# Optimization experiments

Hardware: AMD Instinct MI355X
Metric: run time of the kernel (lower is better)

The kernel has to match this reference:

```python
import jax, jax.numpy as jnp
import numpy as np
from jax import lax

D_MODEL = 768
EXPAND = 2
D_INNER = D_MODEL * EXPAND  # 1536
N_STATE = 16
DT_RANK = D_INNER // 16  # 96
K_CONV = 4
B, L = 2, 1024


def setup_inputs() -> dict:
    key = jax.random.key(0)
    ks = jax.random.split(key, 20)
    s = lambda i, shape, scale=0.02: jax.random.normal(ks[i], shape, dtype=jnp.float32) * scale
    # dt_proj bias init (inverse softplus of dt in [0.001, 0.1])
    def dt_bias(k):
        dt = jnp.exp(jax.random.uniform(k, (D_INNER,)) * (np.log(0.1) - np.log(0.001)) + np.log(0.001))
        return dt + jnp.log(-jnp.expm1(-dt))
    A_log = jnp.log(jnp.arange(1, N_STATE + 1, dtype=jnp.float32))[None, :] * jnp.ones((D_INNER, 1), jnp.float32)
    inp = {
        "u": jax.random.normal(ks[0], (B, L, D_MODEL), dtype=jnp.float32),
        "norm_w": jnp.ones((D_MODEL,), jnp.float32),
        "norm_b": jnp.zeros((D_MODEL,), jnp.float32),
        "fwd_in_w": s(1, (2 * D_INNER, D_MODEL)),
        "fwd_conv_w": s(2, (D_INNER, 1, K_CONV), 0.1),
        "fwd_conv_b": jnp.zeros((D_INNER,), jnp.float32),
        "fwd_A_log": A_log,
        "fwd_xproj_w": s(3, (DT_RANK + 2 * N_STATE, D_INNER)),
        "fwd_dt_w": s(4, (D_INNER, DT_RANK)),
        "fwd_dt_b": dt_bias(ks[5]),
        "fwd_D": jnp.ones((D_INNER,), jnp.float32),
        "bwd_in_w": s(6, (2 * D_INNER, D_MODEL)),
        "bwd_conv_w": s(7, (D_INNER, 1, K_CONV), 0.1),
        "bwd_conv_b": jnp.zeros((D_INNER,), jnp.float32),
        "bwd_A_log": A_log,
        "bwd_xproj_w": s(8, (DT_RANK + 2 * N_STATE, D_INNER)),
        "bwd_dt_w": s(9, (D_INNER, DT_RANK)),
        "bwd_dt_b": dt_bias(ks[10]),
        "bwd_D": jnp.ones((D_INNER,), jnp.float32),
        "out_w": s(11, (D_MODEL, 2 * D_INNER)),
    }
    return inp


def _layernorm(x, w, b, eps=1e-5):
    mu = jnp.mean(x, axis=-1, keepdims=True)
    var = jnp.mean(jnp.square(x - mu), axis=-1, keepdims=True)
    return (x - mu) * lax.rsqrt(var + eps) * w + b


def _dw_causal_conv(x, w, b):
    # x: (B, L, D); torch Conv1d(pad=k-1, groups=D) then trim to L == left-pad causal conv
    xc = jnp.transpose(x, (0, 2, 1))  # (B, D, L)
    y = lax.conv_general_dilated(xc, w, window_strides=(1,),
                                 padding=[(K_CONV - 1, 0)],
                                 feature_group_count=D_INNER,
                                 dimension_numbers=('NCH', 'OIH', 'NCH'))
    return jnp.transpose(y + b[None, :, None], (0, 2, 1))


def _ssm(x, A_log, xproj_w, dt_w, dt_b, Dp):
    # x: (B, L, D)
    x_dbl = x @ xproj_w.T  # (B, L, dt_rank + 2N)
    dt_raw = x_dbl[..., :DT_RANK]
    B_sel = x_dbl[..., DT_RANK:DT_RANK + N_STATE]   # (B, L, N)
    C_sel = x_dbl[..., DT_RANK + N_STATE:]           # (B, L, N)
    dt = jax.nn.softplus(dt_raw @ dt_w.T + dt_b)      # (B, L, D)
    A = -jnp.exp(A_log)                               # (D, N)
    A_bar = jnp.exp(dt[..., None] * A)                # (B, L, D, N)
    Bu = (dt * x)[..., None] * B_sel[:, :, None, :]   # (B, L, D, N)
    # linear recurrence h_t = A_bar_t * h_{t-1} + Bu_t via associative scan
    def combine(c1, c2):
        a1, b1 = c1
        a2, b2 = c2
        return a1 * a2, a2 * b1 + b2
    _, h = lax.associative_scan(combine, (A_bar, Bu), axis=1)
    y = jnp.einsum('bldn,bln->bld', h, C_sel)
    return y + x * Dp


def _branch(u, in_w, conv_w, conv_b, A_log, xproj_w, dt_w, dt_b, Dp, reverse):
    if reverse:
        u = u[:, ::-1]
    xz = u @ in_w.T
    x, z = xz[..., :D_INNER], xz[..., D_INNER:]
    x = jax.nn.silu(_dw_causal_conv(x, conv_w, conv_b))
    x = _ssm(x, A_log, xproj_w, dt_w, dt_b, Dp)
    x = x * jax.nn.silu(z)
    if reverse:
        x = x[:, ::-1]
    return x


def reference(u, norm_w, norm_b,
              fwd_in_w, fwd_conv_w, fwd_conv_b, fwd_A_log, fwd_xproj_w, fwd_dt_w, fwd_dt_b, fwd_D,
              bwd_in_w, bwd_conv_w, bwd_conv_b, bwd_A_log, bwd_xproj_w, bwd_dt_w, bwd_dt_b, bwd_D,
              out_w):
    residual = u
    un = _layernorm(u, norm_w, norm_b)
    x_fwd = _branch(un, fwd_in_w, fwd_conv_w, fwd_conv_b, fwd_A_log, fwd_xproj_w, fwd_dt_w, fwd_dt_b, fwd_D, False)
    x_bwd = _branch(un, bwd_in_w, bwd_conv_w, bwd_conv_b, bwd_A_log, bwd_xproj_w, bwd_dt_w, bwd_dt_b, bwd_D, True)
    x = jnp.concatenate([x_fwd, x_bwd], axis=-1) @ out_w.T
    return x + residual
```

## Files before the change

kernel.cpp:

```cpp
#include <hip/hip_runtime.h>
#include <hip/hip_bf16.h>

#define D_MODEL 768
#define D_INNER 1536
#define N_STATE 16
#define DT_RANK 96
#define KCONV   4
#define Bv      2
#define Lv      1024
#define MROWS   (Bv*Lv)
#define CH      128
#define G       (Lv/CH)
#define PADL    68

typedef __attribute__((ext_vector_type(8))) short bf16x8;
typedef __attribute__((ext_vector_type(4))) float f32x4;

__device__ __forceinline__ void gll16(const void* g, void* l) {
    __builtin_amdgcn_global_load_lds(
        (const __attribute__((address_space(1))) void*)g,
        (__attribute__((address_space(3))) void*)l, 16, 0, 0);
}

__device__ __forceinline__ unsigned short f2bf(float f) {
    unsigned u = __builtin_bit_cast(unsigned, f);
    u += 0x7fffu + ((u >> 16) & 1u);
    return (unsigned short)(u >> 16);
}

template<int CTRL>
__device__ __forceinline__ float dpp_ror_add(float v) {
    int vi = __builtin_bit_cast(int, v);
    int mv = __builtin_amdgcn_update_dpp(vi, vi, CTRL, 0xf, 0xf, true);
    return v + __builtin_bit_cast(float, mv);
}

__global__ __launch_bounds__(256)
void ln_kernel(const float* __restrict__ u, const float* __restrict__ w,
               const float* __restrict__ bvec, unsigned short* __restrict__ o)
{
    int row = blockIdx.x;
    const float* x = u + (size_t)row * D_MODEL;
    int t = threadIdx.x;
    float v0 = x[t], v1 = x[t + 256], v2 = x[t + 512];
    float s  = v0 + v1 + v2;
    float s2 = v0*v0 + v1*v1 + v2*v2;
    for (int off = 32; off; off >>= 1) {
        s  += __shfl_down(s, off);
        s2 += __shfl_down(s2, off);
    }
    __shared__ float rs[4], rs2[4];
    __shared__ float mu_s, rstd_s;
    int wid = t >> 6, lane = t & 63;
    if (lane == 0) { rs[wid] = s; rs2[wid] = s2; }
    __syncthreads();
    if (t == 0) {
        float S  = rs[0] + rs[1] + rs[2] + rs[3];
        float S2 = rs2[0] + rs2[1] + rs2[2] + rs2[3];
        float mu = S / (float)D_MODEL;
        float var = S2 / (float)D_MODEL - mu * mu;
        mu_s = mu;
        rstd_s = rsqrtf(var + 1e-5f);
    }
    __syncthreads();
    float mu = mu_s, r = rstd_s;
    unsigned short* orow = o + (size_t)row * D_MODEL;
    orow[t]       = f2bf((v0 - mu) * r * w[t]       + bvec[t]);
    orow[t + 256] = f2bf((v1 - mu) * r * w[t + 256] + bvec[t + 256]);
    orow[t + 512] = f2bf((v2 - mu) * r * w[t + 512] + bvec[t + 512]);
}

__global__ __launch_bounds__(256)
void f2b(const float* __restrict__ in, unsigned short* __restrict__ o, int n4)
{
    int i = blockIdx.x * 256 + threadIdx.x;
    if (i < n4) {
        float4 v = ((const float4*)in)[i];
        ushort4 r;
        r.x = f2bf(v.x); r.y = f2bf(v.y); r.z = f2bf(v.z); r.w = f2bf(v.w);
        ((ushort4*)o)[i] = r;
    }
}

__global__ __launch_bounds__(256)
void gemm_mfma(const unsigned short* __restrict__ A, int lda, int revA, int Lr,
               const unsigned short* __restrict__ W,
               const float* __restrict__ bias, int act,
               const float* __restrict__ res,
               float* __restrict__ C,
               int M, int N, int K)
{
    __shared__ unsigned short As[128 * 32];
    __shared__ unsigned short Bs[128 * 32];
    const int tid = threadIdx.x;
    const int m0 = blockIdx.y * 128, n0 = blockIdx.x * 128;
    const int lane = tid & 63;
    const int w  = tid >> 6;
    const int wr = w >> 1, wc = w & 1;
    const int lm = lane & 15, lk = lane >> 4;

    const int srow = tid >> 2;
    const int skq  = (tid & 3) * 8;
    int arow0 = m0 + srow, arow1 = m0 + srow + 64;
    if (revA) {
        arow0 = (arow0 / Lr) * Lr + (Lr - 1 - arow0 % Lr);
        arow1 = (arow1 / Lr) * Lr + (Lr - 1 - arow1 % Lr);
    }
    const unsigned short* a0 = A + (size_t)arow0 * lda + skq;
    const unsigned short* a1 = A + (size_t)arow1 * lda + skq;
    const unsigned short* w0 = W + (size_t)(n0 + srow) * K + skq;
    const unsigned short* w1 = W + (size_t)(n0 + srow + 64) * K + skq;

    f32x4 acc[4][4] = {};

    for (int k0 = 0; k0 < K; k0 += 32) {
        __syncthreads();
        gll16(a0 + k0, &As[tid * 8]);
        gll16(a1 + k0, &As[2048 + tid * 8]);
        gll16(w0 + k0, &Bs[tid * 8]);
        gll16(w1 + k0, &Bs[2048 + tid * 8]);
        __syncthreads();

        bf16x8 af[4], bfr[4];
        #pragma unroll
        for (int i = 0; i < 4; i++) {
            af[i]  = *(const bf16x8*)&As[(wr * 64 + i * 16 + lm) * 32 + lk * 8];
            bfr[i] = *(const bf16x8*)&Bs[(wc * 64 + i * 16 + lm) * 32 + lk * 8];
        }
        #pragma unroll
        for (int i = 0; i < 4; i++)
            #pragma unroll
            for (int j = 0; j < 4; j++)
                acc[i][j] = __builtin_amdgcn_mfma_f32_16x16x32_bf16(af[i], bfr[j], acc[i][j], 0, 0, 0);
    }

    #pragma unroll
    for (int i = 0; i < 4; i++) {
        #pragma unroll
        for (int j = 0; j < 4; j++) {
            int row = m0 + wr * 64 + i * 16 + lk * 4;
            int col = n0 + wc * 64 + j * 16 + lm;
            #pragma unroll
            for (int r = 0; r < 4; r++) {
                float v = acc[i][j][r];
                if (bias) v += bias[col];
                if (act == 2) v = (v > 20.f) ? v : log1pf(__expf(v));
                if (res)  v += res[(size_t)(row + r) * N + col];
                C[(size_t)(row + r) * N + col] = v;
            }
        }
    }
}

__global__ __launch_bounds__(256)
void conv_silu(const float* __restrict__ xz, const float* __restrict__ w,
               const float* __restrict__ bias, float* __restrict__ xo,
               unsigned short* __restrict__ xbf)
{
    int t  = blockIdx.x * 256 + threadIdx.x;
    int d  = t % D_INNER;
    int lc = (t / D_INNER) % (Lv / 8);
    int b  = t / (D_INNER * (Lv / 8));
    int l0 = lc * 8;
    const float* src = xz + (size_t)b * Lv * (2 * D_INNER) + d;
    float w0 = w[d*4], w1 = w[d*4+1], w2 = w[d*4+2], w3 = w[d*4+3];
    float bb = bias[d];
    float v[11];
    #pragma unroll
    for (int j = 0; j < 11; j++) {
        int l = l0 - 3 + j;
        v[j] = (l >= 0) ? src[(size_t)l * (2 * D_INNER)] : 0.f;
    }
    size_t base = ((size_t)b * Lv + l0) * D_INNER + d;
    #pragma unroll
    for (int j = 0; j < 8; j++) {
        float a = bb + w0*v[j] + w1*v[j+1] + w2*v[j+2] + w3*v[j+3];
        a = a / (1.f + __expf(-a));
        xo[base + (size_t)j * D_INNER] = a;
        xbf[base + (size_t)j * D_INNER] = f2bf(a);
    }
}

__global__ __launch_bounds__(128)
void scan1(const float* __restrict__ xF, float* __restrict__ dtF,
           const float* __restrict__ xdF, const float* __restrict__ AlF,
           const float* __restrict__ DFp,
           const float* __restrict__ xB, float* __restrict__ dtB,
           const float* __restrict__ xdB, const float* __restrict__ AlB,
           const float* __restrict__ DBp,
           float* __restrict__ y_loc, float* __restrict__ h_end)
{
    const int br = blockIdx.z;
    const int bb = blockIdx.y >> 3, g = blockIdx.y & 7;
    const int d0 = blockIdx.x * 8;

    const float* x    = br ? xB  : xF;
    float*       dtp  = br ? dtB : dtF;
    const float* xd   = br ? xdB : xdF;
    const float* Alog = br ? AlB : AlF;
    const float* Dp   = br ? DBp : DFp;

    __shared__ float xs [2][8][PADL];
    __shared__ float dls[2][8][PADL];
    __shared__ float Bss[2][16][PADL];
    __shared__ float Css[2][16][PADL];

    const int t = threadIdx.x;
    const int n = t & 15, dloc = t >> 4;

    const float* xg  = x   + ((size_t)bb * Lv + g * CH) * D_INNER + d0;
    float*       dtg = dtp + ((size_t)bb * Lv + g * CH) * D_INNER + d0;
    const float* bcg = xd  + ((size_t)bb * Lv + g * CH) * 128;

    const int sl = t >> 1, sdq = (t & 1) * 4;
    const int bl0 = t >> 2,         bq0 = (t & 3) * 4;
    const int bl1 = (t + 128) >> 2, bq1 = ((t + 128) & 3) * 4;

    f32x4 rx, rdt, rb0, rb1, rc0, rc1;

    #define LOADG1(c) do {                                                       \
        int l0_ = (c) * 64;                                                      \
        rx  = *(const f32x4*)(xg  + (size_t)(l0_ + sl) * D_INNER + sdq);         \
        rdt = *(const f32x4*)(dtg + (size_t)(l0_ + sl) * D_INNER + sdq);         \
        rb0 = *(const f32x4*)(bcg + (size_t)(l0_ + bl0) * 128 + DT_RANK           + bq0); \
        rb1 = *(const f32x4*)(bcg + (size_t)(l0_ + bl1) * 128 + DT_RANK           + bq1); \
        rc0 = *(const f32x4*)(bcg + (size_t)(l0_ + bl0) * 128 + DT_RANK + N_STATE + bq0); \
        rc1 = *(const f32x4*)(bcg + (size_t)(l0_ + bl1) * 128 + DT_RANK + N_STATE + bq1); \
    } while (0)

    #define WRITEL1(p) do {                                                      \
        _Pragma("unroll")                                                        \
        for (int j = 0; j < 4; j++) {                                            \
            xs [p][sdq+j][sl] = rx[j];                                           \
            dls[p][sdq+j][sl] = rdt[j];                                          \
            Bss[p][bq0+j][bl0] = rb0[j];                                         \
            Bss[p][bq1+j][bl1] = rb1[j];                                         \
            Css[p][bq0+j][bl0] = rc0[j];                                         \
            Css[p][bq1+j][bl1] = rc1[j];                                         \
        }                                                                        \
    } while (0)

    const float An = -__expf(Alog[(d0 + dloc) * N_STATE + n]);
    const float Dd = Dp[d0 + dloc];
    float h = 0.f, srun = 0.f;

    LOADG1(0);
    WRITEL1(0);
    __syncthreads();

    for (int c = 0; c < 2; ++c) {
        const int p = c;
        if (c == 0) LOADG1(1);

        float yq[4] = {}, Sq[4] = {};
        #pragma unroll
        for (int gg = 0; gg < 16; ++gg) {
            f32x4 xv  = *(const f32x4*)&xs [p][dloc][gg*4];
            f32x4 dtv = *(const f32x4*)&dls[p][dloc][gg*4];
            f32x4 bv  = *(const f32x4*)&Bss[p][n][gg*4];
            f32x4 cv  = *(const f32x4*)&Css[p][n][gg*4];
            #pragma unroll
            for (int j = 0; j < 4; ++j) {
                const int l = gg * 4 + j;
                float dtl = dtv[j];
                float ab = __expf(dtl * An);
                h = fmaf(ab, h, dtl * xv[j] * bv[j]);
                srun += dtl;
                float contrib = h * cv[j];
                contrib = dpp_ror_add<0x121>(contrib);
                contrib = dpp_ror_add<0x122>(contrib);
                contrib = dpp_ror_add<0x124>(contrib);
                contrib = dpp_ror_add<0x128>(contrib);
                float y = contrib + xv[j] * Dd;
                if ((l & 15) == n) { yq[l >> 4] = y; Sq[l >> 4] = srun; }
            }
        }
        if (c == 0) WRITEL1(1);

        #pragma unroll
        for (int q = 0; q < 4; ++q) {
            int lc2 = c * 64 + q * 16 + n;
            int gl  = g * CH + lc2;
            y_loc[((size_t)(br*Bv + bb) * Lv + gl) * D_INNER + d0 + dloc] = yq[q];
            dtg[(size_t)lc2 * D_INNER + dloc] = Sq[q];
        }
        __syncthreads();
    }
    h_end[(((size_t)(br*Bv + bb) * G + g) * D_INNER + d0 + dloc) * 16 + n] = h;
    #undef LOADG1
    #undef WRITEL1
}

__global__ __launch_bounds__(256)
void scan2(const float* __restrict__ SF, const float* __restrict__ SB,
           const float* __restrict__ AlF, const float* __restrict__ AlB,
           const float* __restrict__ h_end, float* __restrict__ h0buf)
{
    int idx = blockIdx.x * 256 + threadIdx.x;
    int n = idx & 15;
    int rest = idx >> 4;
    int d  = rest % D_INNER;
    int bbr = rest / D_INNER;
    int bb = bbr & 1, br = bbr >> 1;

    const float* S    = br ? SB  : SF;
    const float* Alog = br ? AlB : AlF;
    float An = -__expf(Alog[d * N_STATE + n]);

    float h0 = 0.f;
    #pragma unroll
    for (int g = 0; g < G; ++g) {
        size_t base = (((size_t)(br*Bv + bb) * G + g) * D_INNER + d) * 16 + n;
        h0buf[base] = h0;
        float Send = S[((size_t)bb * Lv + g * CH + CH - 1) * D_INNER + d];
        h0 = __expf(An * Send) * h0 + h_end[base];
    }
}

__global__ __launch_bounds__(128)
void scan3(const float* __restrict__ SF, const float* __restrict__ xdF,
           const float* __restrict__ xzF, const float* __restrict__ AlF,
           const float* __restrict__ SB, const float* __restrict__ xdB,
           const float* __restrict__ xzB, const float* __restrict__ AlB,
           const float* __restrict__ y_loc, const float* __restrict__ h0buf,
           unsigned short* __restrict__ ycat)
{
    const int br = blockIdx.z;
    const int bb = blockIdx.y >> 3, g = blockIdx.y & 7;
    const int d0 = blockIdx.x * 8;

    const float* S    = br ? SB  : SF;
    const float* xd   = br ? xdB : xdF;
    const float* xz   = br ? xzB : xzF;
    const float* Alog = br ? AlB : AlF;

    __shared__ float Ss [2][8][PADL];
    __shared__ float zs [2][8][PADL];
    __shared__ float ys [2][8][PADL];
    __shared__ float Css[2][16][PADL];

    const int t = threadIdx.x;
    const int n = t & 15, dloc = t >> 4;

    const float* Sg  = S  + ((size_t)bb * Lv + g * CH) * D_INNER + d0;
    const float* zg  = xz + ((size_t)bb * Lv + g * CH) * (2*D_INNER) + D_INNER + d0;
    const float* yg  = y_loc + ((size_t)(br*Bv + bb) * Lv + g * CH) * D_INNER + d0;
    const float* bcg = xd + ((size_t)bb * Lv + g * CH) * 128;

    const int sl = t >> 1, sdq = (t & 1) * 4;
    const int bl0 = t >> 2,         bq0 = (t & 3) * 4;
    const int bl1 = (t + 128) >> 2, bq1 = ((t + 128) & 3) * 4;

    f32x4 rS, rz, ry, rc0, rc1;

    #define LOADG3(c) do {                                                       \
        int l0_ = (c) * 64;                                                      \
        rS = *(const f32x4*)(Sg + (size_t)(l0_ + sl) * D_INNER + sdq);           \
        rz = *(const f32x4*)(zg + (size_t)(l0_ + sl) * (2*D_INNER) + sdq);       \
        ry = *(const f32x4*)(yg + (size_t)(l0_ + sl) * D_INNER + sdq);           \
        rc0 = *(const f32x4*)(bcg + (size_t)(l0_ + bl0) * 128 + DT_RANK + N_STATE + bq0); \
        rc1 = *(const f32x4*)(bcg + (size_t)(l0_ + bl1) * 128 + DT_RANK + N_STATE + bq1); \
    } while (0)

    #define WRITEL3(p) do {                                                      \
        _Pragma("unroll")                                                        \
        for (int j = 0; j < 4; j++) {                                            \
            Ss[p][sdq+j][sl] = rS[j];                                            \
            zs[p][sdq+j][sl] = rz[j];                                            \
            ys[p][sdq+j][sl] = ry[j];                                            \
            Css[p][bq0+j][bl0] = rc0[j];                                         \
            Css[p][bq1+j][bl1] = rc1[j];                                         \
        }                                                                        \
    } while (0)

    const float An = -__expf(Alog[(d0 + dloc) * N_STATE + n]);
    const float h0 = h0buf[(((size_t)(br*Bv + bb) * G + g) * D_INNER + d0 + dloc) * 16 + n];

    LOADG3(0);
    WRITEL3(0);
    __syncthreads();

    for (int c = 0; c < 2; ++c) {
        const int p = c;
        if (c == 0) LOADG3(1);

        float yq[4] = {};
        #pragma unroll
        for (int gg = 0; gg < 16; ++gg) {
            f32x4 Sv = *(const f32x4*)&Ss [p][dloc][gg*4];
            f32x4 zv = *(const f32x4*)&zs [p][dloc][gg*4];
            f32x4 yv = *(const f32x4*)&ys [p][dloc][gg*4];
            f32x4 cv = *(const f32x4*)&Css[p][n][gg*4];
            #pragma unroll
            for (int j = 0; j < 4; ++j) {
                const int l = gg * 4 + j;
                float corr = cv[j] * __expf(An * Sv[j]) * h0;
                corr = dpp_ror_add<0x121>(corr);
                corr = dpp_ror_add<0x122>(corr);
                corr = dpp_ror_add<0x124>(corr);
                corr = dpp_ror_add<0x128>(corr);
                float y = yv[j] + corr;
                y *= zv[j] * __builtin_amdgcn_rcpf(1.f + __expf(-zv[j]));
                if ((l & 15) == n) yq[l >> 4] = y;
            }
        }
        if (c == 0) WRITEL3(1);

        #pragma unroll
        for (int q = 0; q < 4; ++q) {
            int gl = g * CH + c * 64 + q * 16 + n;
            int lo = br ? (Lv - 1 - gl) : gl;
            ycat[((size_t)bb * Lv + lo) * (2*D_INNER) + br * D_INNER + d0 + dloc] = f2bf(yq[q]);
        }
        __syncthreads();
    }
    #undef LOADG3
    #undef WRITEL3
}

extern "C" void kernel_launch(void* const* d_in, const int* in_sizes, int n_in,
                              void* d_out, int out_size, void* d_ws, size_t ws_size,
                              hipStream_t stream)
{
    (void)in_sizes; (void)n_in; (void)out_size; (void)ws_size;
    const float* u        = (const float*)d_in[0];
    const float* norm_w   = (const float*)d_in[1];
    const float* norm_b   = (const float*)d_in[2];
    const float* f_in_w   = (const float*)d_in[3];
    const float* f_conv_w = (const float*)d_in[4];
    const float* f_conv_b = (const float*)d_in[5];
    const float* f_Alog   = (const float*)d_in[6];
    const float* f_xproj  = (const float*)d_in[7];
    const float* f_dt_w   = (const float*)d_in[8];
    const float* f_dt_b   = (const float*)d_in[9];
    const float* f_D      = (const float*)d_in[10];
    const float* b_in_w   = (const float*)d_in[11];
    const float* b_conv_w = (const float*)d_in[12];
    const float* b_conv_b = (const float*)d_in[13];
    const float* b_Alog   = (const float*)d_in[14];
    const float* b_xproj  = (const float*)d_in[15];
    const float* b_dt_w   = (const float*)d_in[16];
    const float* b_dt_b   = (const float*)d_in[17];
    const float* b_D      = (const float*)d_in[18];
    const float* out_w    = (const float*)d_in[19];
    float* out = (float*)d_out;

    float* p = (float*)d_ws;
    unsigned short* un_bf = (unsigned short*)p;  p += (size_t)MROWS * D_MODEL;
    float* xz_f   = p;  p += (size_t)MROWS * 2 * D_INNER;
    float* xz_b   = p;  p += (size_t)MROWS * 2 * D_INNER;
    float* x_f    = p;  p += (size_t)MROWS * D_INNER;
    float* x_b    = p;  p += (size_t)MROWS * D_INNER;
    unsigned short* xbf_f = (unsigned short*)p;  p += (size_t)MROWS * D_INNER / 2;
    unsigned short* xbf_b = (unsigned short*)p;  p += (size_t)MROWS * D_INNER / 2;
    float* xdbl_f = p;  p += (size_t)MROWS * 128;
    float* xdbl_b = p;  p += (size_t)MROWS * 128;
    float* dt_f   = p;  p += (size_t)MROWS * D_INNER;
    float* dt_b_  = p;  p += (size_t)MROWS * D_INNER;
    unsigned short* yc_bf = (unsigned short*)p;  p += (size_t)MROWS * D_INNER;
    unsigned short* fw_bf = (unsigned short*)p;  p += (size_t)D_INNER * D_MODEL;
    unsigned short* bw_bf = (unsigned short*)p;  p += (size_t)D_INNER * D_MODEL;
    unsigned short* xwf_bf = (unsigned short*)p; p += (size_t)64 * D_INNER;
    unsigned short* xwb_bf = (unsigned short*)p; p += (size_t)64 * D_INNER;
    unsigned short* ow_bf = (unsigned short*)p;  p += (size_t)D_MODEL * D_INNER;
    float* y_loc  = p;  p += (size_t)2 * MROWS * D_INNER;
    float* h_end  = p;  p += (size_t)2 * Bv * G * D_INNER * N_STATE;
    float* h0buf  = p;  p += (size_t)2 * Bv * G * D_INNER * N_STATE;
    unsigned short* xdbf_f = (unsigned short*)p; p += (size_t)MROWS * 128 / 2;
    unsigned short* xdbf_b = (unsigned short*)p; p += (size_t)MROWS * 128 / 2;
    unsigned short* dtwf_bf = (unsigned short*)p; p += (size_t)D_INNER * DT_RANK / 2;
    unsigned short* dtwb_bf = (unsigned short*)p; p += (size_t)D_INNER * DT_RANK / 2;

    ln_kernel<<<MROWS, 256, 0, stream>>>(u, norm_w, norm_b, un_bf);

    f2b<<<(2*D_INNER*D_MODEL/4 + 255)/256, 256, 0, stream>>>(f_in_w, fw_bf, 2*D_INNER*D_MODEL/4);
    f2b<<<(2*D_INNER*D_MODEL/4 + 255)/256, 256, 0, stream>>>(b_in_w, bw_bf, 2*D_INNER*D_MODEL/4);
    f2b<<<(128*D_INNER/4 + 255)/256, 256, 0, stream>>>(f_xproj, xwf_bf, 128*D_INNER/4);
    f2b<<<(128*D_INNER/4 + 255)/256, 256, 0, stream>>>(b_xproj, xwb_bf, 128*D_INNER/4);
    f2b<<<(D_MODEL*2*D_INNER/4 + 255)/256, 256, 0, stream>>>(out_w, ow_bf, D_MODEL*2*D_INNER/4);
    f2b<<<(D_INNER*DT_RANK/4 + 255)/256, 256, 0, stream>>>(f_dt_w, dtwf_bf, D_INNER*DT_RANK/4);
    f2b<<<(D_INNER*DT_RANK/4 + 255)/256, 256, 0, stream>>>(b_dt_w, dtwb_bf, D_INNER*DT_RANK/4);

    gemm_mfma<<<dim3(2*D_INNER/128, MROWS/128), 256, 0, stream>>>(
        un_bf, D_MODEL, 0, Lv, fw_bf, nullptr, 0, nullptr, xz_f, MROWS, 2*D_INNER, D_MODEL);
    gemm_mfma<<<dim3(2*D_INNER/128, MROWS/128), 256, 0, stream>>>(
        un_bf, D_MODEL, 1, Lv, bw_bf, nullptr, 0, nullptr, xz_b, MROWS, 2*D_INNER, D_MODEL);

    int convBlocks = (Bv * (Lv/8) * D_INNER) / 256;
    conv_silu<<<convBlocks, 256, 0, stream>>>(xz_f, f_conv_w, f_conv_b, x_f, xbf_f);
    conv_silu<<<convBlocks, 256, 0, stream>>>(xz_b, b_conv_w, b_conv_b, x_b, xbf_b);

    gemm_mfma<<<dim3(1, MROWS/128), 256, 0, stream>>>(
        xbf_f, D_INNER, 0, Lv, xwf_bf, nullptr, 0, nullptr, xdbl_f, MROWS, 128, D_INNER);
    gemm_mfma<<<dim3(1, MROWS/128), 256, 0, stream>>>(
        xbf_b, D_INNER, 0, Lv, xwb_bf, nullptr, 0, nullptr, xdbl_b, MROWS, 128, D_INNER);

    f2b<<<(MROWS*128/4 + 255)/256, 256, 0, stream>>>(xdbl_f, xdbf_f, MROWS*128/4);
    f2b<<<(MROWS*128/4 + 255)/256, 256, 0, stream>>>(xdbl_b, xdbf_b, MROWS*128/4);
    gemm_mfma<<<dim3(D_INNER/128, MROWS/128), 256, 0, stream>>>(
        xdbf_f, 128, 0, Lv, dtwf_bf, f_dt_b, 2, nullptr, dt_f, MROWS, D_INNER, DT_RANK);
    gemm_mfma<<<dim3(D_INNER/128, MROWS/128), 256, 0, stream>>>(
        xdbf_b, 128, 0, Lv, dtwb_bf, b_dt_b, 2, nullptr, dt_b_, MROWS, D_INNER, DT_RANK);

    scan1<<<dim3(D_INNER/8, Bv*G, 2), 128, 0, stream>>>(
        x_f, dt_f, xdbl_f, f_Alog, f_D,
        x_b, dt_b_, xdbl_b, b_Alog, b_D, y_loc, h_end);
    scan2<<<(2*Bv*D_INNER*N_STATE)/256, 256, 0, stream>>>(
        dt_f, dt_b_, f_Alog, b_Alog, h_end, h0buf);
    scan3<<<dim3(D_INNER/8, Bv*G, 2), 128, 0, stream>>>(
        dt_f, xdbl_f, xz_f, f_Alog,
        dt_b_, xdbl_b, xz_b, b_Alog, y_loc, h0buf, yc_bf);

    gemm_mfma<<<dim3(D_MODEL/128, MROWS/128), 256, 0, stream>>>(
        yc_bf, 2*D_INNER, 0, Lv, ow_bf, nullptr, 0, u, out, MROWS, D_MODEL, 2*D_INNER);
}
```

Baseline: 622.9 us.

## Recompute chunk scan in pass three instead of storing local outputs

```diff
diff --git a/kernel.cpp b/kernel.cpp
--- a/kernel.cpp
+++ b/kernel.cpp
@@ -181,67 +181,58 @@
     }
 }
 
-__global__ __launch_bounds__(128)
-void scan1(const float* __restrict__ xF, float* __restrict__ dtF,
+__global__ __launch_bounds__(128, 6)
+void scan1(const float* __restrict__ xF, const float* __restrict__ dtF,
            const float* __restrict__ xdF, const float* __restrict__ AlF,
-           const float* __restrict__ DFp,
-           const float* __restrict__ xB, float* __restrict__ dtB,
+           const float* __restrict__ xB, const float* __restrict__ dtB,
            const float* __restrict__ xdB, const float* __restrict__ AlB,
-           const float* __restrict__ DBp,
-           float* __restrict__ y_loc, float* __restrict__ h_end)
+           float* __restrict__ h_end, float* __restrict__ Send)
 {
     const int br = blockIdx.z;
     const int bb = blockIdx.y >> 3, g = blockIdx.y & 7;
     const int d0 = blockIdx.x * 8;
 
     const float* x    = br ? xB  : xF;
-    float*       dtp  = br ? dtB : dtF;
+    const float* dt   = br ? dtB : dtF;
     const float* xd   = br ? xdB : xdF;
     const float* Alog = br ? AlB : AlF;
-    const float* Dp   = br ? DBp : DFp;
 
     __shared__ float xs [2][8][PADL];
     __shared__ float dls[2][8][PADL];
     __shared__ float Bss[2][16][PADL];
-    __shared__ float Css[2][16][PADL];
 
     const int t = threadIdx.x;
     const int n = t & 15, dloc = t >> 4;
 
-    const float* xg  = x   + ((size_t)bb * Lv + g * CH) * D_INNER + d0;
-    float*       dtg = dtp + ((size_t)bb * Lv + g * CH) * D_INNER + d0;
-    const float* bcg = xd  + ((size_t)bb * Lv + g * CH) * 128;
+    const float* xg  = x  + ((size_t)bb * Lv + g * CH) * D_INNER + d0;
+    const float* dtg = dt + ((size_t)bb * Lv + g * CH) * D_INNER + d0;
+    const float* bcg = xd + ((size_t)bb * Lv + g * CH) * 128;
 
     const int sl = t >> 1, sdq = (t & 1) * 4;
     const int bl0 = t >> 2,         bq0 = (t & 3) * 4;
     const int bl1 = (t + 128) >> 2, bq1 = ((t + 128) & 3) * 4;
 
-    f32x4 rx, rdt, rb0, rb1, rc0, rc1;
+    f32x4 rx, rdt, rb0, rb1;
 
     #define LOADG1(c) do {                                                       \
         int l0_ = (c) * 64;                                                      \
         rx  = *(const f32x4*)(xg  + (size_t)(l0_ + sl) * D_INNER + sdq);         \
         rdt = *(const f32x4*)(dtg + (size_t)(l0_ + sl) * D_INNER + sdq);         \
-        rb0 = *(const f32x4*)(bcg + (size_t)(l0_ + bl0) * 128 + DT_RANK           + bq0); \
-        rb1 = *(const f32x4*)(bcg + (size_t)(l0_ + bl1) * 128 + DT_RANK           + bq1); \
-        rc0 = *(const f32x4*)(bcg + (size_t)(l0_ + bl0) * 128 + DT_RANK + N_STATE + bq0); \
-        rc1 = *(const f32x4*)(bcg + (size_t)(l0_ + bl1) * 128 + DT_RANK + N_STATE + bq1); \
+        rb0 = *(const f32x4*)(bcg + (size_t)(l0_ + bl0) * 128 + DT_RANK + bq0);  \
+        rb1 = *(const f32x4*)(bcg + (size_t)(l0_ + bl1) * 128 + DT_RANK + bq1);  \
     } while (0)
 
-    #define WRITEL1(p) do {                                                      \
-        _Pragma("unroll")                                                        \
-        for (int j = 0; j < 4; j++) {                                            \
-            xs [p][sdq+j][sl] = rx[j];                                           \
-            dls[p][sdq+j][sl] = rdt[j];                                          \
-            Bss[p][bq0+j][bl0] = rb0[j];                                         \
-            Bss[p][bq1+j][bl1] = rb1[j];                                         \
-            Css[p][bq0+j][bl0] = rc0[j];                                         \
-            Css[p][bq1+j][bl1] = rc1[j];                                         \
-        }                                                                        \
+    #define WRITEL1(p) do {                                                     \
+        _Pragma("unroll")                                                       \
+        for (int j = 0; j < 4; j++) {                                           \
+            xs [p][sdq+j][sl] = rx[j];                                          \
+            dls[p][sdq+j][sl] = rdt[j];                                         \
+            Bss[p][bq0+j][bl0] = rb0[j];                                        \
+            Bss[p][bq1+j][bl1] = rb1[j];                                        \
+        }                                                                       \
     } while (0)
 
     const float An = -__expf(Alog[(d0 + dloc) * N_STATE + n]);
-    const float Dd = Dp[d0 + dloc];
     float h = 0.f, srun = 0.f;
 
     LOADG1(0);
@@ -252,47 +243,30 @@
         const int p = c;
         if (c == 0) LOADG1(1);
 
-        float yq[4] = {}, Sq[4] = {};
         #pragma unroll
         for (int gg = 0; gg < 16; ++gg) {
             f32x4 xv  = *(const f32x4*)&xs [p][dloc][gg*4];
             f32x4 dtv = *(const f32x4*)&dls[p][dloc][gg*4];
             f32x4 bv  = *(const f32x4*)&Bss[p][n][gg*4];
-            f32x4 cv  = *(const f32x4*)&Css[p][n][gg*4];
             #pragma unroll
             for (int j = 0; j < 4; ++j) {
-                const int l = gg * 4 + j;
-                float dtl = dtv[j];
-                float ab = __expf(dtl * An);
-                h = fmaf(ab, h, dtl * xv[j] * bv[j]);
-                srun += dtl;
-                float contrib = h * cv[j];
-                contrib = dpp_ror_add<0x121>(contrib);
-                contrib = dpp_ror_add<0x122>(contrib);
-                contrib = dpp_ror_add<0x124>(contrib);
-                contrib = dpp_ror_add<0x128>(contrib);
-                float y = contrib + xv[j] * Dd;
-                if ((l & 15) == n) { yq[l >> 4] = y; Sq[l >> 4] = srun; }
+                float ab = __expf(dtv[j] * An);
+                h = fmaf(ab, h, dtv[j] * xv[j] * bv[j]);
+                srun += dtv[j];
             }
         }
-        if (c == 0) WRITEL1(1);
-
-        #pragma unroll
-        for (int q = 0; q < 4; ++q) {
-            int lc2 = c * 64 + q * 16 + n;
-            int gl  = g * CH + lc2;
-            y_loc[((size_t)(br*Bv + bb) * Lv + gl) * D_INNER + d0 + dloc] = yq[q];
-            dtg[(size_t)lc2 * D_INNER + dloc] = Sq[q];
-        }
+        if (c == 0) { WRITEL1(1); }
         __syncthreads();
     }
     h_end[(((size_t)(br*Bv + bb) * G + g) * D_INNER + d0 + dloc) * 16 + n] = h;
+    if (n == 0)
+        Send[((size_t)(br*Bv + bb) * G + g) * D_INNER + d0 + dloc] = srun;
     #undef LOADG1
     #undef WRITEL1
 }
 
 __global__ __launch_bounds__(256)
-void scan2(const float* __restrict__ SF, const float* __restrict__ SB,
+void scan2(const float* __restrict__ Send,
            const float* __restrict__ AlF, const float* __restrict__ AlB,
            const float* __restrict__ h_end, float* __restrict__ h0buf)
 {
@@ -303,7 +277,6 @@
     int bbr = rest / D_INNER;
     int bb = bbr & 1, br = bbr >> 1;
 
-    const float* S    = br ? SB  : SF;
     const float* Alog = br ? AlB : AlF;
     float An = -__expf(Alog[d * N_STATE + n]);
 
@@ -312,69 +285,78 @@
     for (int g = 0; g < G; ++g) {
         size_t base = (((size_t)(br*Bv + bb) * G + g) * D_INNER + d) * 16 + n;
         h0buf[base] = h0;
-        float Send = S[((size_t)bb * Lv + g * CH + CH - 1) * D_INNER + d];
-        h0 = __expf(An * Send) * h0 + h_end[base];
-    }
-}
-
-__global__ __launch_bounds__(128)
-void scan3(const float* __restrict__ SF, const float* __restrict__ xdF,
-           const float* __restrict__ xzF, const float* __restrict__ AlF,
-           const float* __restrict__ SB, const float* __restrict__ xdB,
-           const float* __restrict__ xzB, const float* __restrict__ AlB,
-           const float* __restrict__ y_loc, const float* __restrict__ h0buf,
-           unsigned short* __restrict__ ycat)
+        float Se = Send[((size_t)(br*Bv + bb) * G + g) * D_INNER + d];
+        h0 = __expf(An * Se) * h0 + h_end[base];
+    }
+}
+
+__global__ __launch_bounds__(128, 4)
+void scan3(const float* __restrict__ xF, const float* __restrict__ dtF,
+           const float* __restrict__ xdF, const float* __restrict__ xzF,
+           const float* __restrict__ AlF, const float* __restrict__ DFp,
+           const float* __restrict__ xB, const float* __restrict__ dtB,
+           const float* __restrict__ xdB, const float* __restrict__ xzB,
+           const float* __restrict__ AlB, const float* __restrict__ DBp,
+           const float* __restrict__ h0buf, unsigned short* __restrict__ ycat)
 {
     const int br = blockIdx.z;
     const int bb = blockIdx.y >> 3, g = blockIdx.y & 7;
     const int d0 = blockIdx.x * 8;
 
-    const float* S    = br ? SB  : SF;
+    const float* x    = br ? xB  : xF;
+    const float* dt   = br ? dtB : dtF;
     const float* xd   = br ? xdB : xdF;
     const float* xz   = br ? xzB : xzF;
     const float* Alog = br ? AlB : AlF;
-
-    __shared__ float Ss [2][8][PADL];
+    const float* Dp   = br ? DBp : DFp;
+
+    __shared__ float xs [2][8][PADL];
+    __shared__ float dls[2][8][PADL];
     __shared__ float zs [2][8][PADL];
-    __shared__ float ys [2][8][PADL];
+    __shared__ float Bss[2][16][PADL];
     __shared__ float Css[2][16][PADL];
 
     const int t = threadIdx.x;
     const int n = t & 15, dloc = t >> 4;
 
-    const float* Sg  = S  + ((size_t)bb * Lv + g * CH) * D_INNER + d0;
+    const float* xg  = x  + ((size_t)bb * Lv + g * CH) * D_INNER + d0;
+    const float* dtg = dt + ((size_t)bb * Lv + g * CH) * D_INNER + d0;
     const float* zg  = xz + ((size_t)bb * Lv + g * CH) * (2*D_INNER) + D_INNER + d0;
-    const float* yg  = y_loc + ((size_t)(br*Bv + bb) * Lv + g * CH) * D_INNER + d0;
     const float* bcg = xd + ((size_t)bb * Lv + g * CH) * 128;
 
     const int sl = t >> 1, sdq = (t & 1) * 4;
     const int bl0 = t >> 2,         bq0 = (t & 3) * 4;
     const int bl1 = (t + 128) >> 2, bq1 = ((t + 128) & 3) * 4;
 
-    f32x4 rS, rz, ry, rc0, rc1;
+    f32x4 rx, rdt, rz, rb0, rb1, rc0, rc1;
 
     #define LOADG3(c) do {                                                       \
         int l0_ = (c) * 64;                                                      \
-        rS = *(const f32x4*)(Sg + (size_t)(l0_ + sl) * D_INNER + sdq);           \
-        rz = *(const f32x4*)(zg + (size_t)(l0_ + sl) * (2*D_INNER) + sdq);       \
-        ry = *(const f32x4*)(yg + (size_t)(l0_ + sl) * D_INNER + sdq);           \
+        rx  = *(const f32x4*)(xg  + (size_t)(l0_ + sl) * D_INNER + sdq);         \
+        rdt = *(const f32x4*)(dtg + (size_t)(l0_ + sl) * D_INNER + sdq);         \
+        rz  = *(const f32x4*)(zg  + (size_t)(l0_ + sl) * (2*D_INNER) + sdq);     \
+        rb0 = *(const f32x4*)(bcg + (size_t)(l0_ + bl0) * 128 + DT_RANK           + bq0); \
+        rb1 = *(const f32x4*)(bcg + (size_t)(l0_ + bl1) * 128 + DT_RANK           + bq1); \
         rc0 = *(const f32x4*)(bcg + (size_t)(l0_ + bl0) * 128 + DT_RANK + N_STATE + bq0); \
         rc1 = *(const f32x4*)(bcg + (size_t)(l0_ + bl1) * 128 + DT_RANK + N_STATE + bq1); \
     } while (0)
 
-    #define WRITEL3(p) do {                                                      \
-        _Pragma("unroll")                                                        \
-        for (int j = 0; j < 4; j++) {                                            \
-            Ss[p][sdq+j][sl] = rS[j];                                            \
-            zs[p][sdq+j][sl] = rz[j];                                            \
-            ys[p][sdq+j][sl] = ry[j];                                            \
-            Css[p][bq0+j][bl0] = rc0[j];                                         \
-            Css[p][bq1+j][bl1] = rc1[j];                                         \
-        }                                                                        \
+    #define WRITEL3(p) do {                                                     \
+        _Pragma("unroll")                                                       \
+        for (int j = 0; j < 4; j++) {                                           \
+            xs [p][sdq+j][sl] = rx[j];                                          \
+            dls[p][sdq+j][sl] = rdt[j];                                         \
+            zs [p][sdq+j][sl] = rz[j];                                          \
+            Bss[p][bq0+j][bl0] = rb0[j];                                        \
+            Bss[p][bq1+j][bl1] = rb1[j];                                        \
+            Css[p][bq0+j][bl0] = rc0[j];                                        \
+            Css[p][bq1+j][bl1] = rc1[j];                                        \
+        }                                                                       \
     } while (0)
 
     const float An = -__expf(Alog[(d0 + dloc) * N_STATE + n]);
-    const float h0 = h0buf[(((size_t)(br*Bv + bb) * G + g) * D_INNER + d0 + dloc) * 16 + n];
+    const float Dd = Dp[d0 + dloc];
+    float h = h0buf[(((size_t)(br*Bv + bb) * G + g) * D_INNER + d0 + dloc) * 16 + n];
 
     LOADG3(0);
     WRITEL3(0);
@@ -387,24 +369,27 @@
         float yq[4] = {};
         #pragma unroll
         for (int gg = 0; gg < 16; ++gg) {
-            f32x4 Sv = *(const f32x4*)&Ss [p][dloc][gg*4];
-            f32x4 zv = *(const f32x4*)&zs [p][dloc][gg*4];
-            f32x4 yv = *(const f32x4*)&ys [p][dloc][gg*4];
-            f32x4 cv = *(const f32x4*)&Css[p][n][gg*4];
+            f32x4 xv  = *(const f32x4*)&xs [p][dloc][gg*4];
+            f32x4 dtv = *(const f32x4*)&dls[p][dloc][gg*4];
+            f32x4 zv  = *(const f32x4*)&zs [p][dloc][gg*4];
+            f32x4 bv  = *(const f32x4*)&Bss[p][n][gg*4];
+            f32x4 cv  = *(const f32x4*)&Css[p][n][gg*4];
             #pragma unroll
             for (int j = 0; j < 4; ++j) {
                 const int l = gg * 4 + j;
-                float corr = cv[j] * __expf(An * Sv[j]) * h0;
-                corr = dpp_ror_add<0x121>(corr);
-                corr = dpp_ror_add<0x122>(corr);
-                corr = dpp_ror_add<0x124>(corr);
-                corr = dpp_ror_add<0x128>(corr);
-                float y = yv[j] + corr;
-                y *= zv[j] * __builtin_amdgcn_rcpf(1.f + __expf(-zv[j]));
+                float ab = __expf(dtv[j] * An);
+                h = fmaf(ab, h, dtv[j] * xv[j] * bv[j]);
+                float contrib = h * cv[j];
+                contrib = dpp_ror_add<0x121>(contrib);
+                contrib = dpp_ror_add<0x122>(contrib);
+                contrib = dpp_ror_add<0x124>(contrib);
+                contrib = dpp_ror_add<0x128>(contrib);
+                float y = (contrib + xv[j] * Dd)
+                        * (zv[j] * __builtin_amdgcn_rcpf(1.f + __expf(-zv[j])));
                 if ((l & 15) == n) yq[l >> 4] = y;
             }
         }
-        if (c == 0) WRITEL3(1);
+        if (c == 0) { WRITEL3(1); }
 
         #pragma unroll
         for (int q = 0; q < 4; ++q) {
@@ -463,9 +448,9 @@
     unsigned short* xwf_bf = (unsigned short*)p; p += (size_t)64 * D_INNER;
     unsigned short* xwb_bf = (unsigned short*)p; p += (size_t)64 * D_INNER;
     unsigned short* ow_bf = (unsigned short*)p;  p += (size_t)D_MODEL * D_INNER;
-    float* y_loc  = p;  p += (size_t)2 * MROWS * D_INNER;
     float* h_end  = p;  p += (size_t)2 * Bv * G * D_INNER * N_STATE;
     float* h0buf  = p;  p += (size_t)2 * Bv * G * D_INNER * N_STATE;
+    float* Send   = p;  p += (size_t)2 * Bv * G * D_INNER;
     unsigned short* xdbf_f = (unsigned short*)p; p += (size_t)MROWS * 128 / 2;
     unsigned short* xdbf_b = (unsigned short*)p; p += (size_t)MROWS * 128 / 2;
     unsigned short* dtwf_bf = (unsigned short*)p; p += (size_t)D_INNER * DT_RANK / 2;
@@ -503,13 +488,13 @@
         xdbf_b, 128, 0, Lv, dtwb_bf, b_dt_b, 2, nullptr, dt_b_, MROWS, D_INNER, DT_RANK);
 
     scan1<<<dim3(D_INNER/8, Bv*G, 2), 128, 0, stream>>>(
-        x_f, dt_f, xdbl_f, f_Alog, f_D,
-        x_b, dt_b_, xdbl_b, b_Alog, b_D, y_loc, h_end);
+        x_f, dt_f, xdbl_f, f_Alog,
+        x_b, dt_b_, xdbl_b, b_Alog, h_end, Send);
     scan2<<<(2*Bv*D_INNER*N_STATE)/256, 256, 0, stream>>>(
-        dt_f, dt_b_, f_Alog, b_Alog, h_end, h0buf);
+        Send, f_Alog, b_Alog, h_end, h0buf);
     scan3<<<dim3(D_INNER/8, Bv*G, 2), 128, 0, stream>>>(
-        dt_f, xdbl_f, xz_f, f_Alog,
-        dt_b_, xdbl_b, xz_b, b_Alog, y_loc, h0buf, yc_bf);
+        x_f, dt_f, xdbl_f, xz_f, f_Alog, f_D,
+        x_b, dt_b_, xdbl_b, xz_b, b_Alog, b_D, h0buf, yc_bf);
 
     gemm_mfma<<<dim3(D_MODEL/128, MROWS/128), 256, 0, stream>>>(
         yc_bf, 2*D_INNER, 0, Lv, ow_bf, nullptr, 0, u, out, MROWS, D_MODEL, 2*D_INNER);
```

New measurement: 570.8 us. 8.4% less time.
